# Kernel tuning notes

Hardware: AMD Instinct MI355X
Metric: run time of the kernel (lower is better)

## Reference

```python
import jax, jax.numpy as jnp
import numpy as np

PATCH = 3
STYLE_STRIDE = 1
SYNTH_STRIDE = 1


def _extract_patches(img, p, stride):
    # img: [1, C, H, W] -> flattened patches [N, C*p*p], row-major over (i, j),
    # matching torch's patches_sampling (channel-major, then kh, kw within a patch).
    pat = jax.lax.conv_general_dilated_patches(img, (p, p), (stride, stride), 'VALID')
    # pat: [1, C*p*p, oh, ow] with feature ordering (C, kh, kw)
    _, cpp, oh, ow = pat.shape
    return jnp.transpose(pat, (0, 2, 3, 1)).reshape(oh * ow, cpp)


def setup_inputs() -> dict:
    key = jax.random.key(0)
    k1, k2 = jax.random.split(key)
    input = jax.random.normal(k1, (1, 256, 96, 96), dtype=jnp.float32)
    target = jax.random.normal(k2, (1, 256, 96, 96), dtype=jnp.float32)
    return {"input": input, "target": target}


def reference(input, target):
    # Style patches (constructor: patches_sampling(target) with mrf_style_stride)
    style = _extract_patches(target, PATCH, STYLE_STRIDE)      # [S, D]
    # Synthesis patches with mrf_synthesis_stride
    synth = _extract_patches(input, PATCH, SYNTH_STRIDE)       # [Q, D]

    # Per-style-patch L2 norm (cal_patches_norm)
    style_norm = jnp.sqrt(jnp.sum(style * style, axis=1))      # [S]

    # conv2d(input, style_patches, stride) == patch dot products: [Q, S]
    resp = jnp.einsum('qd,sd->qs', synth, style)
    resp = resp / style_norm[None, :]

    # argmax over style patches per synthesis location (nearest-neighbor retrieval)
    nn_idx = jnp.argmax(resp, axis=1)                          # [Q]

    # gathered MSE: mean over patch elems, summed over Q, divided by Q -> mean
    diff = synth - style[nn_idx]                               # [Q, D]
    loss = jnp.mean(jnp.mean(diff * diff, axis=1))
    return loss
```

## Files before the change

kernel.cpp:

```cpp
#include <hip/hip_runtime.h>
#include <math.h>

#define NP 8836
#define PW 94
#define IW 96
#define CH 256
#define NTILE 70
#define KT2 18
#define NWG (NTILE * NTILE)
#define NPIX 9216
#define GTS 9216

typedef int   i32x4  __attribute__((ext_vector_type(4)));
typedef int   i32x8  __attribute__((ext_vector_type(8)));
typedef float f32x16 __attribute__((ext_vector_type(16)));

__device__ __forceinline__ unsigned int ordf(float f) {
  unsigned int u = __float_as_uint(f);
  return (u & 0x80000000u) ? ~u : (u | 0x80000000u);
}

__device__ __forceinline__ float blo(unsigned int x) {
  return __uint_as_float(x << 16);
}
__device__ __forceinline__ float bhi(unsigned int x) {
  return __uint_as_float(x & 0xFFFF0000u);
}

typedef const __attribute__((address_space(1))) void GvoidC;
typedef __attribute__((address_space(3))) void Lvoid;
__device__ __forceinline__ void gl16(const void* g, void* l) {
  __builtin_amdgcn_global_load_lds((GvoidC*)g, (Lvoid*)l, 16, 0, 0);
}

__global__ __launch_bounds__(256) void prep_kernel(
    const float* __restrict__ inA, const float* __restrict__ inB,
    unsigned int* __restrict__ TA, unsigned int* __restrict__ TB) {
  __shared__ float tile[64][65];
  int bid = blockIdx.x;
  const float* src; unsigned int* dst;
  if (bid < 576) { src = inA; dst = TA; }
  else           { src = inB; dst = TB; bid -= 576; }
  int cT  = bid & 3;
  int xyT = bid >> 2;
  int t = threadIdx.x;
  int l = t & 63, h = t >> 6;

  #pragma unroll
  for (int i = 0; i < 16; ++i) {
    int c = h * 16 + i;
    tile[c][l] = src[(size_t)(cT * 64 + c) * (IW * IW) + xyT * 64 + l];
  }
  __syncthreads();
  int cu = t & 15;
  #pragma unroll
  for (int i = 0; i < 4; ++i) {
    int xy = (t >> 4) + i * 16;
    int c = cu * 4;
    unsigned int v = __builtin_amdgcn_cvt_pk_fp8_f32(tile[c][xy],     tile[c + 1][xy], 0, false);
    v              = __builtin_amdgcn_cvt_pk_fp8_f32(tile[c + 2][xy], tile[c + 3][xy], v, true);
    dst[(size_t)(xyT * 64 + xy) * 64 + cT * 16 + cu] = v;
  }
}

__global__ void norms_kernel(const unsigned int* __restrict__ TA, const unsigned int* __restrict__ TB,
                             float* __restrict__ rnormS, float* __restrict__ normS,
                             float* __restrict__ normsqS, float* __restrict__ synsq) {
  int wid  = blockIdx.x * 4 + (threadIdx.x >> 6);
  int lane = threadIdx.x & 63;
  bool isStyle = wid < NP;
  int p = isStyle ? wid : wid - NP;
  if (p >= NP) return;
  const unsigned int* T = isStyle ? TB : TA;
  int pi = p / PW, pj = p % PW;
  float s = 0.f;
  #pragma unroll
  for (int kh = 0; kh < 3; ++kh) {
    #pragma unroll
    for (int kw = 0; kw < 3; ++kw) {
      unsigned int v = T[(size_t)((pi + kh) * IW + (pj + kw)) * 64 + lane];
      float f0 = __builtin_amdgcn_cvt_f32_fp8(v, 0);
      float f1 = __builtin_amdgcn_cvt_f32_fp8(v, 1);
      float f2 = __builtin_amdgcn_cvt_f32_fp8(v, 2);
      float f3 = __builtin_amdgcn_cvt_f32_fp8(v, 3);
      s += f0 * f0 + f1 * f1 + f2 * f2 + f3 * f3;
    }
  }
  #pragma unroll
  for (int m = 32; m >= 1; m >>= 1) s += __shfl_xor(s, m, 64);
  if (lane == 0) {
    if (isStyle) {
      normsqS[p] = s;
      float n = sqrtf(s);
      normS[p]  = n;
      rnormS[p] = 1.f / n;
    } else {
      synsq[p] = s;
    }
  }
}

__device__ __forceinline__ i32x8 ldfrag(const unsigned char* rowp, int o0, int o1) {
  i32x4 lo = *(const i32x4*)(rowp + o0);
  i32x4 hi = *(const i32x4*)(rowp + o1);
  return __builtin_shufflevector(lo, hi, 0, 1, 2, 3, 4, 5, 6, 7);
}

__global__ __launch_bounds__(256, 2) void g_gemm_kernel(
    const unsigned char* __restrict__ TA, const unsigned char* __restrict__ TB,
    unsigned short* __restrict__ GT) {
  __shared__ unsigned char As[128 * 128];
  __shared__ unsigned char Bs[128 * 128];

  int orig = blockIdx.x;
  int pid = (orig & 7) * 648 + (orig >> 3);
  int yt = pid % 72, xt = pid / 72;
  int y0 = yt * 128, x0 = xt * 128;
  int t = threadIdx.x, lane = t & 63, wave = t >> 6;
  int wm = wave >> 1, wn = wave & 1;

  int rr = t >> 3;
  int qc = (t & 7) ^ (rr & 7);
  const unsigned char* gA[4];
  const unsigned char* gB[4];
  #pragma unroll
  for (int i = 0; i < 4; ++i) {
    gA[i] = TB + (size_t)(y0 + 32 * i + rr) * CH + qc * 16;
    gB[i] = TA + (size_t)(x0 + 32 * i + rr) * CH + qc * 16;
  }
  unsigned char* lA = As + t * 16;
  unsigned char* lB = Bs + t * 16;

  f32x16 acc[2][2];
  #pragma unroll
  for (int mi = 0; mi < 2; ++mi)
    #pragma unroll
    for (int ni = 0; ni < 2; ++ni)
      #pragma unroll
      for (int j = 0; j < 16; ++j) acc[mi][ni][j] = 0.f;

  int kq = lane >> 5, sw = lane & 7;
  const unsigned char* Arow = As + (size_t)(wm * 64 + (lane & 31)) * 128;
  const unsigned char* Brow = Bs + (size_t)(wn * 64 + (lane & 31)) * 128;

  #pragma unroll 1
  for (int kt = 0; kt < 2; ++kt) {
    int choff = kt * 128;
    if (kt) __syncthreads();
    #pragma unroll
    for (int i = 0; i < 4; ++i) {
      gl16(gA[i] + choff, lA + i * 4096);
      gl16(gB[i] + choff, lB + i * 4096);
    }
    __syncthreads();
    #pragma unroll
    for (int h = 0; h < 2; ++h) {
      int c0 = 2 * kq + 4 * h;
      int o0 = (c0 ^ sw) * 16, o1 = ((c0 + 1) ^ sw) * 16;
      i32x8 af[2], bf[2];
      #pragma unroll
      for (int mi = 0; mi < 2; ++mi) af[mi] = ldfrag(Arow + mi * 32 * 128, o0, o1);
      #pragma unroll
      for (int ni = 0; ni < 2; ++ni) bf[ni] = ldfrag(Brow + ni * 32 * 128, o0, o1);
      #pragma unroll
      for (int mi = 0; mi < 2; ++mi)
        #pragma unroll
        for (int ni = 0; ni < 2; ++ni)
          acc[mi][ni] = __builtin_amdgcn_mfma_scale_f32_32x32x64_f8f6f4(
              af[mi], bf[ni], acc[mi][ni],
              0, 0, 0, 0x7F7F7F7F, 0, 0x7F7F7F7F);
    }
  }

  int col = lane & 31, half = lane >> 5;
  #pragma unroll
  for (int mi = 0; mi < 2; ++mi) {
    #pragma unroll
    for (int ni = 0; ni < 2; ++ni) {
      size_t ybase = (size_t)(y0 + wm * 64 + mi * 32 + 4 * half);
      size_t xg    = (size_t)(x0 + wn * 64 + ni * 32 + col);
      unsigned short* p = GT + ybase * GTS + xg;
      #pragma unroll
      for (int g = 0; g < 4; ++g)
        #pragma unroll
        for (int j = 0; j < 4; ++j) {
          unsigned int u = __float_as_uint(acc[mi][ni][4 * g + j]);
          unsigned short b = (unsigned short)((u + 0x7FFFu + ((u >> 16) & 1u)) >> 16);
          p[(size_t)(j + 8 * g) * GTS] = b;
        }
    }
  }
}

__global__ __launch_bounds__(768) void tapsum_kernel(
    const unsigned short* __restrict__ GT, const float* __restrict__ rnormS,
    unsigned long long* __restrict__ best) {
  __shared__ unsigned char glds[55296];
  __shared__ unsigned long long sm[16][96];
  __shared__ float rnlds[96];
  int orig = blockIdx.x;
  int xcd = orig & 7, idx = orig >> 3;
  int pid = (xcd < 4 ? xcd * 1105 : 4 * 1105 + (xcd - 4) * 1104) + idx;
  int d = pid / 94, pos = pid - d * 94;
  int qi = pos;
  int si = pos + d; if (si >= 94) si -= 94;

  int t = threadIdx.x;

  const unsigned char* GTb = (const unsigned char*)GT;
  #pragma unroll
  for (int k = 0; k < 5; ++k) {
    int c = k * 768 + t;
    if (c < 3456) {
      int b = c / 1152, rem = c - b * 1152;
      int r = rem / 12, s = rem - r * 12;
      size_t gaddr = ((size_t)((si + b) * 96 + r) * GTS + (size_t)(qi + b) * 96) * 2
                     + (size_t)s * 16;
      gl16(GTb + gaddr, glds + c * 16);
    }
  }
  if (t < 94) rnlds[t] = rnormS[si * 94 + t];
  __syncthreads();

  int u = t >> 1, sub = t & 1;
  if (u < 376) {
    int g = u / 47, p = u - g * 47;
    int sj0 = g * 12 + sub * 6;
    int niter = (g == 7 && sub == 1) ? 4 : 6;
    float bv0 = -3.0e38f, bv1 = -3.0e38f;
    int bs0 = sj0, bs1 = sj0;
    int va0 = sj0 * 192 + 4 * p;
    int va1 = va0 + 18432;
    int va2 = va0 + 36864;
    for (int j = 0; j < niter; ++j) {
      unsigned int d00_0 = *(const unsigned int*)(glds + va0);
      unsigned int d10_0 = *(const unsigned int*)(glds + va0 + 192);
      unsigned int d11_0 = *(const unsigned int*)(glds + va0 + 196);
      unsigned int d21_0 = *(const unsigned int*)(glds + va0 + 388);
      unsigned int d00_1 = *(const unsigned int*)(glds + va1);
      unsigned int d10_1 = *(const unsigned int*)(glds + va1 + 192);
      unsigned int d11_1 = *(const unsigned int*)(glds + va1 + 196);
      unsigned int d21_1 = *(const unsigned int*)(glds + va1 + 388);
      unsigned int d00_2 = *(const unsigned int*)(glds + va2);
      unsigned int d10_2 = *(const unsigned int*)(glds + va2 + 192);
      unsigned int d11_2 = *(const unsigned int*)(glds + va2 + 196);
      unsigned int d21_2 = *(const unsigned int*)(glds + va2 + 388);
      float rn = rnlds[sj0 + j];

      float a0 = (((blo(d00_0) + blo(d21_0)) + bhi(d10_1)) + blo(d00_2)) + blo(d21_2);
      float a1 = ((bhi(d10_0) + blo(d00_1)) + blo(d21_1)) + bhi(d10_2);
      float v0 = (a0 + a1) * rn;
      float a0b = (((bhi(d00_0) + bhi(d21_0)) + blo(d11_1)) + bhi(d00_2)) + bhi(d21_2);
      float a1b = ((blo(d11_0) + bhi(d00_1)) + bhi(d21_1)) + blo(d11_2);
      float v1 = (a0b + a1b) * rn;

      int sj = sj0 + j;
      if (v0 > bv0) { bv0 = v0; bs0 = sj; }
      if (v1 > bv1) { bv1 = v1; bs1 = sj; }
      va0 += 192; va1 += 192; va2 += 192;
    }
    int s0i = si * 94 + bs0;
    unsigned long long cand0 = ((unsigned long long)ordf(bv0) << 32) |
                               (unsigned long long)(0xFFFFFFFFu - (unsigned)s0i);
    int s1i = si * 94 + bs1;
    unsigned long long cand1 = ((unsigned long long)ordf(bv1) << 32) |
                               (unsigned long long)(0xFFFFFFFFu - (unsigned)s1i);
    sm[g * 2 + sub][2 * p]     = cand0;
    sm[g * 2 + sub][2 * p + 1] = cand1;
  }
  __syncthreads();
  if (t < 94) {
    unsigned long long c = sm[0][t];
    #pragma unroll
    for (int r = 1; r < 16; ++r) {
      unsigned long long o = sm[r][t];
      if (o > c) c = o;
    }
    atomicMax(best + (size_t)(qi * 94 + t) * 8, c);
  }
}

__global__ __launch_bounds__(256, 2) void gemm_argmax_kernel(
    const unsigned char* __restrict__ TA, const unsigned char* __restrict__ TB,
    const float* __restrict__ rnormS, unsigned long long* __restrict__ best) {
  __shared__ unsigned char As[128 * 128];
  __shared__ unsigned char Bs[128 * 128];

  int orig = blockIdx.x;
  int xcd = orig & 7, idx = orig >> 3;
  int pid = (xcd < 4 ? xcd * 613 : 4 * 613 + (xcd - 4) * 612) + idx;

  int mt = pid % NTILE, nt = pid / NTILE;
  int q0 = mt * 128, s0 = nt * 128;
  int t = threadIdx.x, lane = t & 63, wave = t >> 6;
  int wm = wave >> 1, wn = wave & 1;

  int rr = t >> 3;
  int qc = (t & 7) ^ (rr & 7);
  const unsigned char* gA[4];
  const unsigned char* gB[4];
  #pragma unroll
  for (int i = 0; i < 4; ++i) {
    int qa = q0 + 32 * i + rr; if (qa > NP - 1) qa = NP - 1;
    int sa = s0 + 32 * i + rr; if (sa > NP - 1) sa = NP - 1;
    gA[i] = TA + (size_t)((qa / PW) * IW + (qa % PW)) * CH + qc * 16;
    gB[i] = TB + (size_t)((sa / PW) * IW + (sa % PW)) * CH + qc * 16;
  }
  unsigned char* lA = As + t * 16;
  unsigned char* lB = Bs + t * 16;

  f32x16 acc[2][2];
  #pragma unroll
  for (int mi = 0; mi < 2; ++mi)
    #pragma unroll
    for (int ni = 0; ni < 2; ++ni)
      #pragma unroll
      for (int j = 0; j < 16; ++j) acc[mi][ni][j] = 0.f;

  int kq = lane >> 5, sw = lane & 7;
  const unsigned char* Arow = As + (size_t)(wm * 64 + (lane & 31)) * 128;
  const unsigned char* Brow = Bs + (size_t)(wn * 64 + (lane & 31)) * 128;

  #pragma unroll 1
  for (int kt = 0; kt < KT2; ++kt) {
    int chunk = kt >> 1;
    int kh = chunk / 3, kw = chunk - kh * 3;
    int choff = (kh * IW + kw) * CH + (kt & 1) * 128;
    if (kt) __syncthreads();
    #pragma unroll
    for (int i = 0; i < 4; ++i) {
      gl16(gA[i] + choff, lA + i * 4096);
      gl16(gB[i] + choff, lB + i * 4096);
    }
    __syncthreads();
    #pragma unroll
    for (int h = 0; h < 2; ++h) {
      int c0 = 2 * kq + 4 * h;
      int o0 = (c0 ^ sw) * 16, o1 = ((c0 + 1) ^ sw) * 16;
      i32x8 af[2], bf[2];
      #pragma unroll
      for (int mi = 0; mi < 2; ++mi) af[mi] = ldfrag(Arow + mi * 32 * 128, o0, o1);
      #pragma unroll
      for (int ni = 0; ni < 2; ++ni) bf[ni] = ldfrag(Brow + ni * 32 * 128, o0, o1);
      #pragma unroll
      for (int mi = 0; mi < 2; ++mi)
        #pragma unroll
        for (int ni = 0; ni < 2; ++ni)
          acc[mi][ni] = __builtin_amdgcn_mfma_scale_f32_32x32x64_f8f6f4(
              af[mi], bf[ni], acc[mi][ni],
              0, 0, 0, 0x7F7F7F7F, 0, 0x7F7F7F7F);
    }
  }

  int col = lane & 31, half = lane >> 5;
  float rn[2]; int sc[2]; bool sv[2];
  #pragma unroll
  for (int ni = 0; ni < 2; ++ni) {
    int s = s0 + wn * 64 + ni * 32 + col;
    sc[ni] = s;
    sv[ni] = (s < NP);
    rn[ni] = sv[ni] ? rnormS[s] : 0.f;
  }
  #pragma unroll
  for (int mi = 0; mi < 2; ++mi) {
    #pragma unroll
    for (int reg = 0; reg < 16; ++reg) {
      unsigned long long p = 0ull;
      #pragma unroll
      for (int ni = 0; ni < 2; ++ni) {
        float v = acc[mi][ni][reg] * rn[ni];
        unsigned long long cand =
            ((unsigned long long)ordf(v) << 32) |
            (unsigned long long)(0xFFFFFFFFu - (unsigned)sc[ni]);
        cand = sv[ni] ? cand : 0ull;
        if (cand > p) p = cand;
      }
      #pragma unroll
      for (int sh = 16; sh >= 1; sh >>= 1) {
        unsigned long long o = __shfl_xor(p, sh, 64);
        if (o > p) p = o;
      }
      int q = q0 + wm * 64 + mi * 32 + (reg & 3) + 8 * (reg >> 2) + 4 * half;
      if (col == 0 && q < NP) atomicMax(best + (size_t)q * 8, p);
    }
  }
}

__global__ __launch_bounds__(256) void finalize_kernel(
    const unsigned long long* __restrict__ best,
    const float* __restrict__ normS,
    const float* __restrict__ normsqS,
    const float* __restrict__ synsq,
    float* __restrict__ out) {
  __shared__ float swv[4];
  int t = threadIdx.x;
  int q = blockIdx.x * 256 + t;
  float a = 0.f;
  if (q < NP) {
    unsigned long long p = best[(size_t)q * 8];
    unsigned int o   = (unsigned int)(p >> 32);
    unsigned int idx = 0xFFFFFFFFu - (unsigned int)(p & 0xFFFFFFFFull);
    unsigned int u   = (o & 0x80000000u) ? (o & 0x7FFFFFFFu) : ~o;
    float resp = __uint_as_float(u);
    float dot  = resp * normS[idx];
    a = (synsq[q] - 2.f * dot + normsqS[idx]) * (1.f / ((float)NP * 2304.f));
  }
  #pragma unroll
  for (int m = 32; m >= 1; m >>= 1) a += __shfl_xor(a, m, 64);
  if ((t & 63) == 0) swv[t >> 6] = a;
  __syncthreads();
  if (t == 0) atomicAdd(out, (swv[0] + swv[1]) + (swv[2] + swv[3]));
}

extern "C" void kernel_launch(void* const* d_in, const int* in_sizes, int n_in,
                              void* d_out, int out_size, void* d_ws, size_t ws_size,
                              hipStream_t stream) {
  const float* inA = (const float*)d_in[0];
  const float* inB = (const float*)d_in[1];
  float* out = (float*)d_out;

  char* ws = (char*)d_ws;
  unsigned char* TA = (unsigned char*)ws;
  unsigned char* TB = (unsigned char*)(ws + 2359296);
  float* rnormS  = (float*)(ws + 4718592);
  float* normS   = (float*)(ws + 4718592 + 35344);
  float* normsqS = (float*)(ws + 4718592 + 70688);
  float* synsq   = (float*)(ws + 4718592 + 106032);
  unsigned long long* best = (unsigned long long*)(ws + 4718592 + 141376);
  const size_t GT_OFF = 4718592ull + 141376ull + 565504ull;
  unsigned short* GT = (unsigned short*)(ws + GT_OFF);
  const size_t NEED = GT_OFF + (size_t)NPIX * NPIX * 2;

  (void)hipMemsetAsync(best, 0, (size_t)NP * 64, stream);
  (void)hipMemsetAsync(out, 0, sizeof(float), stream);
  prep_kernel<<<dim3(1152), dim3(256), 0, stream>>>(inA, inB, (unsigned int*)TA, (unsigned int*)TB);
  norms_kernel<<<dim3((2 * NP + 3) / 4), dim3(256), 0, stream>>>(
      (const unsigned int*)TA, (const unsigned int*)TB, rnormS, normS, normsqS, synsq);
  if (ws_size >= NEED) {
    g_gemm_kernel<<<dim3(72 * 72), dim3(256), 0, stream>>>(TA, TB, GT);
    tapsum_kernel<<<dim3(NP), dim3(768), 0, stream>>>(GT, rnormS, best);
  } else {
    gemm_argmax_kernel<<<dim3(NWG), dim3(256), 0, stream>>>(TA, TB, rnormS, best);
  }
  finalize_kernel<<<dim3(35), dim3(256), 0, stream>>>(best, normS, normsqS, synsq, out);
}
```

Before: 211.6 us.

## Pre-sum the three diagonal tap rows into an fp32 LDS tile in tapsum

The tapsum kernel no longer copies three raw bf16 row blocks into LDS asynchronously. It loads them directly, sums the three diagonal offsets per element, and stores a 96x96 fp32 partial-sum tile. The argmax loop then needs only three LDS reads per candidate instead of twelve, and each thread handles one query with twelve style candidates, so the cross-group reduction shrinks to eight rows. The cost is that the global loads become synchronous 4-byte loads instead of 16-byte async copies, and the floating-point summation order changes, which can alter tie-breaking.

```diff
diff --git a/kernel.cpp b/kernel.cpp
--- a/kernel.cpp
+++ b/kernel.cpp
@@ -195,8 +195,8 @@
 __global__ __launch_bounds__(768) void tapsum_kernel(
     const unsigned short* __restrict__ GT, const float* __restrict__ rnormS,
     unsigned long long* __restrict__ best) {
-  __shared__ unsigned char glds[55296];
-  __shared__ unsigned long long sm[16][96];
+  __shared__ float S[96 * 96];
+  __shared__ unsigned long long sm[8][96];
   __shared__ float rnlds[96];
   int orig = blockIdx.x;
   int xcd = orig & 7, idx = orig >> 3;
@@ -209,70 +209,44 @@
 
   const unsigned char* GTb = (const unsigned char*)GT;
   #pragma unroll
-  for (int k = 0; k < 5; ++k) {
-    int c = k * 768 + t;
-    if (c < 3456) {
-      int b = c / 1152, rem = c - b * 1152;
-      int r = rem / 12, s = rem - r * 12;
-      size_t gaddr = ((size_t)((si + b) * 96 + r) * GTS + (size_t)(qi + b) * 96) * 2
-                     + (size_t)s * 16;
-      gl16(GTb + gaddr, glds + c * 16);
-    }
+  for (int k = 0; k < 6; ++k) {
+    int p2 = t + k * 768;
+    int r = p2 / 48, cp = p2 - r * 48;
+    unsigned int d0 = *(const unsigned int*)(GTb +
+        ((size_t)((si + 0) * 96 + r) * GTS + (size_t)(qi + 0) * 96 + 2 * cp) * 2);
+    unsigned int d1 = *(const unsigned int*)(GTb +
+        ((size_t)((si + 1) * 96 + r) * GTS + (size_t)(qi + 1) * 96 + 2 * cp) * 2);
+    unsigned int d2 = *(const unsigned int*)(GTb +
+        ((size_t)((si + 2) * 96 + r) * GTS + (size_t)(qi + 2) * 96 + 2 * cp) * 2);
+    S[r * 96 + 2 * cp]     = (blo(d0) + blo(d1)) + blo(d2);
+    S[r * 96 + 2 * cp + 1] = (bhi(d0) + bhi(d1)) + bhi(d2);
   }
   if (t < 94) rnlds[t] = rnormS[si * 94 + t];
   __syncthreads();
 
-  int u = t >> 1, sub = t & 1;
-  if (u < 376) {
-    int g = u / 47, p = u - g * 47;
-    int sj0 = g * 12 + sub * 6;
-    int niter = (g == 7 && sub == 1) ? 4 : 6;
-    float bv0 = -3.0e38f, bv1 = -3.0e38f;
-    int bs0 = sj0, bs1 = sj0;
-    int va0 = sj0 * 192 + 4 * p;
-    int va1 = va0 + 18432;
-    int va2 = va0 + 36864;
+  if (t < 752) {
+    int g = t / 94, qj = t - g * 94;
+    int sj0 = g * 12;
+    int niter = (g == 7) ? 10 : 12;
+    float bv = -3.0e38f; int bs = sj0;
+    int base = sj0 * 96 + qj;
     for (int j = 0; j < niter; ++j) {
-      unsigned int d00_0 = *(const unsigned int*)(glds + va0);
-      unsigned int d10_0 = *(const unsigned int*)(glds + va0 + 192);
-      unsigned int d11_0 = *(const unsigned int*)(glds + va0 + 196);
-      unsigned int d21_0 = *(const unsigned int*)(glds + va0 + 388);
-      unsigned int d00_1 = *(const unsigned int*)(glds + va1);
-      unsigned int d10_1 = *(const unsigned int*)(glds + va1 + 192);
-      unsigned int d11_1 = *(const unsigned int*)(glds + va1 + 196);
-      unsigned int d21_1 = *(const unsigned int*)(glds + va1 + 388);
-      unsigned int d00_2 = *(const unsigned int*)(glds + va2);
-      unsigned int d10_2 = *(const unsigned int*)(glds + va2 + 192);
-      unsigned int d11_2 = *(const unsigned int*)(glds + va2 + 196);
-      unsigned int d21_2 = *(const unsigned int*)(glds + va2 + 388);
-      float rn = rnlds[sj0 + j];
-
-      float a0 = (((blo(d00_0) + blo(d21_0)) + bhi(d10_1)) + blo(d00_2)) + blo(d21_2);
-      float a1 = ((bhi(d10_0) + blo(d00_1)) + blo(d21_1)) + bhi(d10_2);
-      float v0 = (a0 + a1) * rn;
-      float a0b = (((bhi(d00_0) + bhi(d21_0)) + blo(d11_1)) + bhi(d00_2)) + bhi(d21_2);
-      float a1b = ((blo(d11_0) + bhi(d00_1)) + bhi(d21_1)) + blo(d11_2);
-      float v1 = (a0b + a1b) * rn;
-
-      int sj = sj0 + j;
-      if (v0 > bv0) { bv0 = v0; bs0 = sj; }
-      if (v1 > bv1) { bv1 = v1; bs1 = sj; }
-      va0 += 192; va1 += 192; va2 += 192;
-    }
-    int s0i = si * 94 + bs0;
-    unsigned long long cand0 = ((unsigned long long)ordf(bv0) << 32) |
-                               (unsigned long long)(0xFFFFFFFFu - (unsigned)s0i);
-    int s1i = si * 94 + bs1;
-    unsigned long long cand1 = ((unsigned long long)ordf(bv1) << 32) |
-                               (unsigned long long)(0xFFFFFFFFu - (unsigned)s1i);
-    sm[g * 2 + sub][2 * p]     = cand0;
-    sm[g * 2 + sub][2 * p + 1] = cand1;
+      float t0 = S[base];
+      float t1 = S[base + 97];
+      float t2 = S[base + 194];
+      float v = ((t0 + t1) + t2) * rnlds[sj0 + j];
+      if (v > bv) { bv = v; bs = sj0 + j; }
+      base += 96;
+    }
+    int sidx = si * 94 + bs;
+    sm[g][qj] = ((unsigned long long)ordf(bv) << 32) |
+                (unsigned long long)(0xFFFFFFFFu - (unsigned)sidx);
   }
   __syncthreads();
   if (t < 94) {
     unsigned long long c = sm[0][t];
     #pragma unroll
-    for (int r = 1; r < 16; ++r) {
+    for (int r = 1; r < 8; ++r) {
       unsigned long long o = sm[r][t];
       if (o > c) c = o;
     }
```

After: 192.7 us. -8.9%, faster.
